# Optimization experiments

Hardware: AMD Instinct MI355X
Metric: run time of the kernel (lower is better)

The kernel has to match this reference:

```python
import jax, jax.numpy as jnp
import numpy as np

NUM_HEADS = 4
DIM_MODEL = 256
DIM_HEAD = DIM_MODEL // NUM_HEADS  # 64


def _conv1x1(w, b, x):
    # Conv1d kernel_size=1: [B, D_in, N] -> [B, D_out, N]
    return jnp.einsum('oi,bin->bon', w, x) + b[None, :, None]


def setup_inputs() -> dict:
    key = jax.random.key(0)
    ks = jax.random.split(key, 12)
    B, D, N = 8, DIM_MODEL, 2048
    s = 1.0 / np.sqrt(D)
    inp = {
        'query': jax.random.normal(ks[0], (B, D, N), dtype=jnp.float32),
        'key': jax.random.normal(ks[1], (B, D, N), dtype=jnp.float32),
        'value': jax.random.normal(ks[2], (B, D, N), dtype=jnp.float32),
        'wq': jax.random.normal(ks[3], (D, D), dtype=jnp.float32) * s,
        'bq': jax.random.normal(ks[4], (D,), dtype=jnp.float32) * 0.01,
        'wk': jax.random.normal(ks[5], (D, D), dtype=jnp.float32) * s,
        'bk': jax.random.normal(ks[6], (D,), dtype=jnp.float32) * 0.01,
        'wv': jax.random.normal(ks[7], (D, D), dtype=jnp.float32) * s,
        'bv': jax.random.normal(ks[8], (D,), dtype=jnp.float32) * 0.01,
        'wm': jax.random.normal(ks[9], (D, D), dtype=jnp.float32) * s,
        'bm': jax.random.normal(ks[10], (D,), dtype=jnp.float32) * 0.01,
    }
    return inp


def reference(query, key, value, wq, bq, wk, bk, wv, bv, wm, bm):
    B = query.shape[0]
    d, h = DIM_HEAD, NUM_HEADS
    # 1x1 conv projections, then split channels as (dim_head, num_heads) per torch view
    q = _conv1x1(wq, bq, query).reshape(B, d, h, -1)  # [B, d, h, N]
    k = _conv1x1(wk, bk, key).reshape(B, d, h, -1)    # [B, d, h, M]
    v = _conv1x1(wv, bv, value).reshape(B, d, h, -1)  # [B, d, h, M]
    norm = 1.0 / float(d) ** 0.5
    scores = jnp.einsum('bdhn,bdhm->bhnm', q, k) * norm  # [B, h, N, M]
    prob = jax.nn.softmax(scores, axis=-1)
    attn = jnp.einsum('bhnm,bdhm->bdhn', prob, v)        # [B, d, h, N]
    out = _conv1x1(wm, bm, attn.reshape(B, d * h, -1))   # [B, D, N]
    return out
```

## Files before the change

kernel.cpp:

```cpp
#include <hip/hip_runtime.h>
#include <math.h>

#define BB 8
#define DD 256
#define NN 2048
#define NH 4
#define DH 64

typedef _Float16 half8   __attribute__((ext_vector_type(8)));
typedef _Float16 half4_t __attribute__((ext_vector_type(4)));
typedef _Float16 half2_t __attribute__((ext_vector_type(2)));
typedef float    floatx4 __attribute__((ext_vector_type(4)));

#define MFMA32(A, B, C) __builtin_amdgcn_mfma_f32_16x16x32_f16(A, B, C, 0, 0, 0)

#define SC 0.18033688011112042f

__global__ __launch_bounds__(256) void prep_weights(
    const float* __restrict__ wq, const float* __restrict__ wk,
    const float* __restrict__ wv, const float* __restrict__ wm,
    _Float16* __restrict__ wqf, _Float16* __restrict__ wkf,
    _Float16* __restrict__ wvf, _Float16* __restrict__ wmf)
{
    int id = blockIdx.x * 256 + threadIdx.x;
    wqf[id] = (_Float16)wq[id];
    wkf[id] = (_Float16)wk[id];
    wvf[id] = (_Float16)wv[id];
    int row = id >> 8, col = id & 255;
    int hh = col >> 6, dd = col & 63;
    wmf[id] = (_Float16)wm[row * 256 + dd * 4 + hh];
}


__global__ __launch_bounds__(256, 3) void conv_qkv(
    const _Float16* __restrict__ wqf, const _Float16* __restrict__ wkf,
    const _Float16* __restrict__ wvf,
    const float* __restrict__ bq, const float* __restrict__ bk,
    const float* __restrict__ bv,
    const float* __restrict__ Xq, const float* __restrict__ Xk,
    const float* __restrict__ Xv,
    _Float16* __restrict__ Yq, _Float16* __restrict__ Yk,
    _Float16* __restrict__ Yv)
{
    const int n0 = blockIdx.x * 64;
    const int b  = blockIdx.y;
    const int zh = blockIdx.z;
    const int z  = zh >> 1;
    const int hf = zh & 1;
    const _Float16* Wf = z == 0 ? wqf : (z == 1 ? wkf : wvf);
    const float* bias  = z == 0 ? bq  : (z == 1 ? bk  : bv);
    const float* X     = z == 0 ? Xq  : (z == 1 ? Xk  : Xv);
    const float osc    = z == 0 ? SC : 1.0f;
    const int cout0 = hf * 128;

    const int t = threadIdx.x;
    const int w = t >> 6, l = t & 63, c = l & 15, q = l >> 4;

    __shared__ _Float16 smem[64 * 264];

    half8 af[2][8];
    {
        const _Float16* wp = Wf + (size_t)(cout0 + w * 32 + c) * 256 + q * 8;
        #pragma unroll
        for (int rt = 0; rt < 2; ++rt)
            #pragma unroll
            for (int ch = 0; ch < 8; ++ch)
                af[rt][ch] = *(const half8*)(wp + rt * 16 * 256 + ch * 32);
    }

    {
        const int nb = t & 15, kb = t >> 4;
        #pragma unroll
        for (int cc = 0; cc < 4; ++cc) {
            const float* Xg = X + (size_t)b * DD * NN +
                              (size_t)(cc * 64 + kb * 4) * NN + n0 + nb * 4;
            float4 x[4];
            #pragma unroll
            for (int i = 0; i < 4; ++i) x[i] = *(const float4*)(Xg + (size_t)i * NN);
            #pragma unroll
            for (int j = 0; j < 4; ++j) {
                half4_t hv;
                #pragma unroll
                for (int i = 0; i < 4; ++i) hv[i] = (_Float16)(((const float*)&x[i])[j]);
                *(half4_t*)(smem + (nb * 4 + j) * 264 + cc * 64 + kb * 4) = hv;
            }
        }
    }
    __syncthreads();

    floatx4 acc[2][4];
    #pragma unroll
    for (int rt = 0; rt < 2; ++rt)
        #pragma unroll
        for (int nt = 0; nt < 4; ++nt) acc[rt][nt] = (floatx4){0.f, 0.f, 0.f, 0.f};

    #pragma unroll
    for (int ch = 0; ch < 8; ++ch)
        #pragma unroll
        for (int nt = 0; nt < 4; ++nt) {
            half8 bx = *(const half8*)(smem + (nt * 16 + c) * 264 + ch * 32 + q * 8);
            acc[0][nt] = MFMA32(af[0][ch], bx, acc[0][nt]);
            acc[1][nt] = MFMA32(af[1][ch], bx, acc[1][nt]);
        }

    if (z < 2) {
        __syncthreads();
        #pragma unroll
        for (int rt = 0; rt < 2; ++rt)
            #pragma unroll
            for (int nt = 0; nt < 4; ++nt) {
                half4_t hv;
                #pragma unroll
                for (int r = 0; r < 4; ++r)
                    hv[r] = (_Float16)((acc[rt][nt][r] +
                            bias[cout0 + w * 32 + rt * 16 + q * 4 + r]) * osc);
                *(half4_t*)(smem + (nt * 16 + c) * 136 + w * 32 + rt * 16 + q * 4) = hv;
            }
        __syncthreads();
        _Float16* Y = z == 0 ? Yq : Yk;
        const int nn = t >> 2, hh = t & 3;
        half8 hv[4];
        #pragma unroll
        for (int i = 0; i < 4; ++i)
            #pragma unroll
            for (int k = 0; k < 8; ++k)
                hv[i][k] = smem[nn * 136 + (i * 8 + k) * 4 + hh];
        _Float16* dst = Y + ((size_t)(b * NH + hh) * NN + n0 + nn) * 64 + hf * 32;
        #pragma unroll
        for (int i = 0; i < 4; ++i) *(half8*)(dst + i * 8) = hv[i];
    } else {
        __syncthreads();
        #pragma unroll
        for (int rt = 0; rt < 2; ++rt)
            #pragma unroll
            for (int nt = 0; nt < 4; ++nt)
                #pragma unroll
                for (int r = 0; r < 4; ++r)
                    smem[(w * 32 + rt * 16 + q * 4 + r) * 72 + nt * 16 + c] =
                        (_Float16)(acc[rt][nt][r] +
                                   bias[cout0 + w * 32 + rt * 16 + q * 4 + r]);
        __syncthreads();
        const int cl = t >> 1, noff = (t & 1) * 32;
        const int cout = cout0 + cl;
        const int hh = cout & 3, dd = cout >> 2;
        _Float16* dst = Yv + ((size_t)(b * NH + hh) * 64 + dd) * NN + n0 + noff;
        #pragma unroll
        for (int i = 0; i < 4; ++i)
            *(half8*)(dst + i * 8) = *(const half8*)(smem + cl * 72 + noff + i * 8);
    }
}

__global__ __launch_bounds__(256, 3) void conv_o(
    const _Float16* __restrict__ Wf, const float* __restrict__ bias,
    const _Float16* __restrict__ At, float* __restrict__ out)
{
    const int n0 = blockIdx.x * 64;
    const int b  = blockIdx.y;
    const int hf = blockIdx.z;
    const int cout0 = hf * 128;

    const int t = threadIdx.x;
    const int w = t >> 6, l = t & 63, c = l & 15, q = l >> 4;

    __shared__ float fs[128 * 66];

    half8 af[2][8];
    {
        const _Float16* wp = Wf + (size_t)(cout0 + w * 32 + c) * 256 + q * 8;
        #pragma unroll
        for (int rt = 0; rt < 2; ++rt)
            #pragma unroll
            for (int ch = 0; ch < 8; ++ch)
                af[rt][ch] = *(const half8*)(wp + rt * 16 * 256 + ch * 32);
    }

    floatx4 acc[2][4];
    #pragma unroll
    for (int rt = 0; rt < 2; ++rt)
        #pragma unroll
        for (int nt = 0; nt < 4; ++nt) acc[rt][nt] = (floatx4){0.f, 0.f, 0.f, 0.f};

    #pragma unroll
    for (int ch = 0; ch < 8; ++ch)
        #pragma unroll
        for (int nt = 0; nt < 4; ++nt) {
            half8 bx = *(const half8*)(At +
                ((size_t)b * NN + n0 + nt * 16 + c) * 256 + ch * 32 + q * 8);
            acc[0][nt] = MFMA32(af[0][ch], bx, acc[0][nt]);
            acc[1][nt] = MFMA32(af[1][ch], bx, acc[1][nt]);
        }

    #pragma unroll
    for (int rt = 0; rt < 2; ++rt)
        #pragma unroll
        for (int nt = 0; nt < 4; ++nt)
            #pragma unroll
            for (int r = 0; r < 4; ++r)
                fs[(w * 32 + rt * 16 + q * 4 + r) * 66 + nt * 16 + c] =
                    acc[rt][nt][r] + bias[cout0 + w * 32 + rt * 16 + q * 4 + r];
    __syncthreads();
    const int cl = t >> 1, noff = (t & 1) * 32;
    float* dst = out + (size_t)b * DD * NN + (size_t)(cout0 + cl) * NN + n0 + noff;
    #pragma unroll
    for (int i = 0; i < 8; ++i)
        *(float4*)(dst + i * 4) = *(const float4*)(fs + cl * 66 + noff + i * 4);
}

__global__ __launch_bounds__(512) void attn_mfma6(
    const _Float16* __restrict__ Qt, const _Float16* __restrict__ Kt,
    const _Float16* __restrict__ V, _Float16* __restrict__ At)
{
    const int n0 = blockIdx.x * 128;
    const int h  = blockIdx.y;
    const int b  = blockIdx.z;
    const int t  = threadIdx.x;
    const int w  = t >> 6, l = t & 63, c = l & 15, q = l >> 4;

    const size_t bh = (size_t)(b * NH + h);

    __shared__ _Float16 smem[9216 + 8704];
    _Float16* Ks = smem;
    _Float16* Vs = smem + 9216;

    half8 bq2[2];
    #pragma unroll
    for (int ch = 0; ch < 2; ++ch)
        bq2[ch] = *(const half8*)(Qt + (bh * NN + n0 + w * 16 + c) * 64 + ch * 32 + q * 8);

    float lp = 0.f;
    floatx4 o[4];
    #pragma unroll
    for (int dt = 0; dt < 4; ++dt) o[dt] = (floatx4){0.f, 0.f, 0.f, 0.f};

    const int ksr = t >> 2, ksc = (t & 3) * 16;
    const int vr  = t >> 3, vcb = (t & 7) * 16;
    const _Float16* Kg = Kt + bh * NN * 64;
    const _Float16* Vg = V + bh * 64 * NN;

    half8 kpre[2], vpre[2];
    kpre[0] = *(const half8*)(Kg + (size_t)ksr * 64 + ksc);
    kpre[1] = *(const half8*)(Kg + (size_t)ksr * 64 + ksc + 8);
    vpre[0] = *(const half8*)(Vg + (size_t)vr * NN + vcb);
    vpre[1] = *(const half8*)(Vg + (size_t)vr * NN + vcb + 8);

    for (int m0 = 0; m0 < NN; m0 += 128) {
        __syncthreads();
        *(half8*)(Ks + ksr * 72 + ksc)     = kpre[0];
        *(half8*)(Ks + ksr * 72 + ksc + 8) = kpre[1];
        #pragma unroll
        for (int u = 0; u < 2; ++u) {
            const int mb = vcb + u * 8;
            const int p0 = (mb & ~31) + (((mb >> 2) & 3) << 3) + (((mb >> 4) & 1) << 2);
            half4_t lo, hi;
            #pragma unroll
            for (int j = 0; j < 4; ++j) { lo[j] = vpre[u][j]; hi[j] = vpre[u][4 + j]; }
            *(half4_t*)(Vs + vr * 136 + p0)     = lo;
            *(half4_t*)(Vs + vr * 136 + p0 + 8) = hi;
        }
        __syncthreads();

        const int mn = (m0 + 128 < NN) ? m0 + 128 : m0;
        kpre[0] = *(const half8*)(Kg + (size_t)(mn + ksr) * 64 + ksc);
        kpre[1] = *(const half8*)(Kg + (size_t)(mn + ksr) * 64 + ksc + 8);
        vpre[0] = *(const half8*)(Vg + (size_t)vr * NN + mn + vcb);
        vpre[1] = *(const half8*)(Vg + (size_t)vr * NN + mn + vcb + 8);

        #pragma unroll
        for (int mt2 = 0; mt2 < 4; ++mt2) {
            half8 p8;
            #pragma unroll
            for (int hfm = 0; hfm < 2; ++hfm) {
                const int mt = mt2 * 2 + hfm;
                floatx4 s = {0.f, 0.f, 0.f, 0.f};
                #pragma unroll
                for (int ch = 0; ch < 2; ++ch) {
                    half8 ak = *(const half8*)(Ks + (mt * 16 + c) * 72 + ch * 32 + q * 8);
                    s = MFMA32(ak, bq2[ch], s);
                }
                float e0 = exp2f(s[0]), e1 = exp2f(s[1]);
                float e2 = exp2f(s[2]), e3 = exp2f(s[3]);
                lp += (e0 + e1) + (e2 + e3);
                half2_t c01 = __builtin_bit_cast(half2_t, __builtin_amdgcn_cvt_pkrtz(e0, e1));
                half2_t c23 = __builtin_bit_cast(half2_t, __builtin_amdgcn_cvt_pkrtz(e2, e3));
                p8[hfm * 4 + 0] = c01[0]; p8[hfm * 4 + 1] = c01[1];
                p8[hfm * 4 + 2] = c23[0]; p8[hfm * 4 + 3] = c23[1];
            }
            #pragma unroll
            for (int dt = 0; dt < 4; ++dt) {
                half8 av = *(const half8*)(Vs + (dt * 16 + c) * 136 + mt2 * 32 + q * 8);
                o[dt] = MFMA32(av, p8, o[dt]);
            }
        }
    }

    lp += __shfl_xor(lp, 16);
    lp += __shfl_xor(lp, 32);
    const float inv = 1.f / lp;

    __syncthreads();
    _Float16* fsm = smem;
    #pragma unroll
    for (int dt = 0; dt < 4; ++dt) {
        half4_t hv;
        #pragma unroll
        for (int r = 0; r < 4; ++r) hv[r] = (_Float16)(o[dt][r] * inv);
        *(half4_t*)(fsm + (w * 16 + c) * 72 + dt * 16 + q * 4) = hv;
    }
    __syncthreads();
    const int rn = t >> 2, seg = (t & 3) * 16;
    _Float16* dst = At + ((size_t)b * NN + n0 + rn) * 256 + h * 64 + seg;
    *(half8*)(dst)     = *(const half8*)(fsm + rn * 72 + seg);
    *(half8*)(dst + 8) = *(const half8*)(fsm + rn * 72 + seg + 8);
}

extern "C" void kernel_launch(void* const* d_in, const int* in_sizes, int n_in,
                              void* d_out, int out_size, void* d_ws, size_t ws_size,
                              hipStream_t stream) {
    const float* query = (const float*)d_in[0];
    const float* key_  = (const float*)d_in[1];
    const float* value = (const float*)d_in[2];
    const float* wq    = (const float*)d_in[3];
    const float* bq    = (const float*)d_in[4];
    const float* wk    = (const float*)d_in[5];
    const float* bk    = (const float*)d_in[6];
    const float* wv    = (const float*)d_in[7];
    const float* bv    = (const float*)d_in[8];
    const float* wm    = (const float*)d_in[9];
    const float* bm    = (const float*)d_in[10];
    float* out = (float*)d_out;

    _Float16* ws = (_Float16*)d_ws;
    _Float16* wqf = ws;
    _Float16* wkf = wqf + 65536;
    _Float16* wvf = wkf + 65536;
    _Float16* wmf = wvf + 65536;
    const size_t e16 = (size_t)BB * NH * NN * DH;
    _Float16* qf = ws + 262144;
    _Float16* kf = qf + e16;
    _Float16* vf = kf + e16;
    _Float16* at = vf + e16;

    prep_weights<<<256, 256, 0, stream>>>(wq, wk, wv, wm, wqf, wkf, wvf, wmf);
    conv_qkv<<<dim3(32, 8, 6), 256, 0, stream>>>(wqf, wkf, wvf, bq, bk, bv,
                                                 query, key_, value, qf, kf, vf);
    attn_mfma6<<<dim3(16, 4, 8), 512, 0, stream>>>(qf, kf, vf, at);
    conv_o<<<dim3(32, 8, 2), 256, 0, stream>>>(wmf, bm, at, out);
}
```

Baseline: 199.1 us.

## Double-buffer attention K/V tiles, swizzle LDS, merge conv_qkv output halves

The attention kernel now double-buffers K/V tiles in shared memory, so each iteration needs one barrier instead of two and staging of the next tile overlaps compute. LDS layouts for K, V and the conv input tile get XOR swizzles to cut bank conflicts on the MFMA operand reads. conv_qkv has each block compute both 128-channel output halves from one staged input tile, halving the input loads and conversions at the cost of half as many blocks. The doubled shared memory in attention may lower occupancy.

Measured after the change: 202.0 us. About the same (+1.5%).

```diff
diff --git a/kernel.cpp b/kernel.cpp
--- a/kernel.cpp
+++ b/kernel.cpp
@@ -31,7 +31,6 @@
     wmf[id] = (_Float16)wm[row * 256 + dd * 4 + hh];
 }
 
-
 __global__ __launch_bounds__(256, 3) void conv_qkv(
     const _Float16* __restrict__ wqf, const _Float16* __restrict__ wkf,
     const _Float16* __restrict__ wvf,
@@ -44,32 +43,24 @@
 {
     const int n0 = blockIdx.x * 64;
     const int b  = blockIdx.y;
-    const int zh = blockIdx.z;
-    const int z  = zh >> 1;
-    const int hf = zh & 1;
+    const int z  = blockIdx.z;
     const _Float16* Wf = z == 0 ? wqf : (z == 1 ? wkf : wvf);
     const float* bias  = z == 0 ? bq  : (z == 1 ? bk  : bv);
     const float* X     = z == 0 ? Xq  : (z == 1 ? Xk  : Xv);
     const float osc    = z == 0 ? SC : 1.0f;
-    const int cout0 = hf * 128;
 
     const int t = threadIdx.x;
     const int w = t >> 6, l = t & 63, c = l & 15, q = l >> 4;
 
-    __shared__ _Float16 smem[64 * 264];
-
-    half8 af[2][8];
-    {
-        const _Float16* wp = Wf + (size_t)(cout0 + w * 32 + c) * 256 + q * 8;
-        #pragma unroll
-        for (int rt = 0; rt < 2; ++rt)
-            #pragma unroll
-            for (int ch = 0; ch < 8; ++ch)
-                af[rt][ch] = *(const half8*)(wp + rt * 16 * 256 + ch * 32);
-    }
+    __shared__ _Float16 smem[64 * 264 + 9216];
+    _Float16* Xs = smem;
+    _Float16* Es = smem + 64 * 264;
+
+    const int gk = (c & 3) << 1;
 
     {
         const int nb = t & 15, kb = t >> 4;
+        const int slot = (kb >> 1), sub = (kb & 1) * 4;
         #pragma unroll
         for (int cc = 0; cc < 4; ++cc) {
             const float* Xg = X + (size_t)b * DD * NN +
@@ -82,71 +73,87 @@
                 half4_t hv;
                 #pragma unroll
                 for (int i = 0; i < 4; ++i) hv[i] = (_Float16)(((const float*)&x[i])[j]);
-                *(half4_t*)(smem + (nb * 4 + j) * 264 + cc * 64 + kb * 4) = hv;
+                *(half4_t*)(Xs + (nb * 4 + j) * 264 +
+                            (((cc * 8 + slot) ^ (j << 1)) << 3) + sub) = hv;
             }
         }
     }
     __syncthreads();
 
-    floatx4 acc[2][4];
-    #pragma unroll
-    for (int rt = 0; rt < 2; ++rt)
-        #pragma unroll
-        for (int nt = 0; nt < 4; ++nt) acc[rt][nt] = (floatx4){0.f, 0.f, 0.f, 0.f};
-
-    #pragma unroll
-    for (int ch = 0; ch < 8; ++ch)
-        #pragma unroll
-        for (int nt = 0; nt < 4; ++nt) {
-            half8 bx = *(const half8*)(smem + (nt * 16 + c) * 264 + ch * 32 + q * 8);
-            acc[0][nt] = MFMA32(af[0][ch], bx, acc[0][nt]);
-            acc[1][nt] = MFMA32(af[1][ch], bx, acc[1][nt]);
-        }
-
-    if (z < 2) {
-        __syncthreads();
+    for (int hf = 0; hf < 2; ++hf) {
+        const int cout0 = hf * 128;
+
+        half8 af[2][8];
+        {
+            const _Float16* wp = Wf + (size_t)(cout0 + w * 32 + c) * 256 + q * 8;
+            #pragma unroll
+            for (int rt = 0; rt < 2; ++rt)
+                #pragma unroll
+                for (int ch = 0; ch < 8; ++ch)
+                    af[rt][ch] = *(const half8*)(wp + rt * 16 * 256 + ch * 32);
+        }
+
+        floatx4 acc[2][4];
         #pragma unroll
         for (int rt = 0; rt < 2; ++rt)
             #pragma unroll
+            for (int nt = 0; nt < 4; ++nt) acc[rt][nt] = (floatx4){0.f, 0.f, 0.f, 0.f};
+
+        #pragma unroll
+        for (int ch = 0; ch < 8; ++ch)
+            #pragma unroll
             for (int nt = 0; nt < 4; ++nt) {
-                half4_t hv;
-                #pragma unroll
-                for (int r = 0; r < 4; ++r)
-                    hv[r] = (_Float16)((acc[rt][nt][r] +
-                            bias[cout0 + w * 32 + rt * 16 + q * 4 + r]) * osc);
-                *(half4_t*)(smem + (nt * 16 + c) * 136 + w * 32 + rt * 16 + q * 4) = hv;
+                half8 bx = *(const half8*)(Xs + (nt * 16 + c) * 264 +
+                                           (((ch * 4 + q) ^ gk) << 3));
+                acc[0][nt] = MFMA32(af[0][ch], bx, acc[0][nt]);
+                acc[1][nt] = MFMA32(af[1][ch], bx, acc[1][nt]);
             }
-        __syncthreads();
-        _Float16* Y = z == 0 ? Yq : Yk;
-        const int nn = t >> 2, hh = t & 3;
-        half8 hv[4];
-        #pragma unroll
-        for (int i = 0; i < 4; ++i)
-            #pragma unroll
-            for (int k = 0; k < 8; ++k)
-                hv[i][k] = smem[nn * 136 + (i * 8 + k) * 4 + hh];
-        _Float16* dst = Y + ((size_t)(b * NH + hh) * NN + n0 + nn) * 64 + hf * 32;
-        #pragma unroll
-        for (int i = 0; i < 4; ++i) *(half8*)(dst + i * 8) = hv[i];
-    } else {
-        __syncthreads();
-        #pragma unroll
-        for (int rt = 0; rt < 2; ++rt)
-            #pragma unroll
-            for (int nt = 0; nt < 4; ++nt)
-                #pragma unroll
-                for (int r = 0; r < 4; ++r)
-                    smem[(w * 32 + rt * 16 + q * 4 + r) * 72 + nt * 16 + c] =
-                        (_Float16)(acc[rt][nt][r] +
-                                   bias[cout0 + w * 32 + rt * 16 + q * 4 + r]);
-        __syncthreads();
-        const int cl = t >> 1, noff = (t & 1) * 32;
-        const int cout = cout0 + cl;
-        const int hh = cout & 3, dd = cout >> 2;
-        _Float16* dst = Yv + ((size_t)(b * NH + hh) * 64 + dd) * NN + n0 + noff;
-        #pragma unroll
-        for (int i = 0; i < 4; ++i)
-            *(half8*)(dst + i * 8) = *(const half8*)(smem + cl * 72 + noff + i * 8);
+
+        if (z < 2) {
+            __syncthreads();
+            #pragma unroll
+            for (int rt = 0; rt < 2; ++rt)
+                #pragma unroll
+                for (int nt = 0; nt < 4; ++nt) {
+                    half4_t hv;
+                    #pragma unroll
+                    for (int r = 0; r < 4; ++r)
+                        hv[r] = (_Float16)((acc[rt][nt][r] +
+                                bias[cout0 + w * 32 + rt * 16 + q * 4 + r]) * osc);
+                    *(half4_t*)(Es + (nt * 16 + c) * 136 + w * 32 + rt * 16 + q * 4) = hv;
+                }
+            __syncthreads();
+            _Float16* Y = z == 0 ? Yq : Yk;
+            const int nn = t >> 2, hh = t & 3;
+            half8 hv[4];
+            #pragma unroll
+            for (int i = 0; i < 4; ++i)
+                #pragma unroll
+                for (int k = 0; k < 8; ++k)
+                    hv[i][k] = Es[nn * 136 + (i * 8 + k) * 4 + hh];
+            _Float16* dst = Y + ((size_t)(b * NH + hh) * NN + n0 + nn) * 64 + hf * 32;
+            #pragma unroll
+            for (int i = 0; i < 4; ++i) *(half8*)(dst + i * 8) = hv[i];
+        } else {
+            __syncthreads();
+            #pragma unroll
+            for (int rt = 0; rt < 2; ++rt)
+                #pragma unroll
+                for (int nt = 0; nt < 4; ++nt)
+                    #pragma unroll
+                    for (int r = 0; r < 4; ++r)
+                        Es[(w * 32 + rt * 16 + q * 4 + r) * 72 + nt * 16 + c] =
+                            (_Float16)(acc[rt][nt][r] +
+                                       bias[cout0 + w * 32 + rt * 16 + q * 4 + r]);
+            __syncthreads();
+            const int cl = t >> 1, noff = (t & 1) * 32;
+            const int cout = cout0 + cl;
+            const int hh = cout & 3, dd = cout >> 2;
+            _Float16* dst = Yv + ((size_t)(b * NH + hh) * 64 + dd) * NN + n0 + noff;
+            #pragma unroll
+            for (int i = 0; i < 4; ++i)
+                *(half8*)(dst + i * 8) = *(const half8*)(Es + cl * 72 + noff + i * 8);
+        }
     }
 }
 
@@ -218,9 +225,7 @@
 
     const size_t bh = (size_t)(b * NH + h);
 
-    __shared__ _Float16 smem[9216 + 8704];
-    _Float16* Ks = smem;
-    _Float16* Vs = smem + 9216;
+    __shared__ _Float16 smem[2 * 17920];
 
     half8 bq2[2];
     #pragma unroll
@@ -236,6 +241,18 @@
     const int vr  = t >> 3, vcb = (t & 7) * 16;
     const _Float16* Kg = Kt + bh * NN * 64;
     const _Float16* Vg = V + bh * 64 * NN;
+
+    const int gk  = (c & 3) << 1;
+    const int rk0 = ((0 + q) ^ gk) << 3;
+    const int rk1 = ((4 + q) ^ gk) << 3;
+    int rv[4];
+    #pragma unroll
+    for (int mt2 = 0; mt2 < 4; ++mt2) rv[mt2] = ((mt2 * 4 + q) ^ gk) << 3;
+    const int gK  = (ksr & 3) << 1;
+    const int s0  = (t & 3) * 2;
+    const int wk0 = (s0 ^ gK) << 3;
+    const int wk1 = ((s0 + 1) ^ gK) << 3;
+    const int gV  = (vr & 3) << 1;
 
     half8 kpre[2], vpre[2];
     kpre[0] = *(const half8*)(Kg + (size_t)ksr * 64 + ksc);
@@ -243,28 +260,46 @@
     vpre[0] = *(const half8*)(Vg + (size_t)vr * NN + vcb);
     vpre[1] = *(const half8*)(Vg + (size_t)vr * NN + vcb + 8);
 
-    for (int m0 = 0; m0 < NN; m0 += 128) {
-        __syncthreads();
-        *(half8*)(Ks + ksr * 72 + ksc)     = kpre[0];
-        *(half8*)(Ks + ksr * 72 + ksc + 8) = kpre[1];
-        #pragma unroll
-        for (int u = 0; u < 2; ++u) {
-            const int mb = vcb + u * 8;
-            const int p0 = (mb & ~31) + (((mb >> 2) & 3) << 3) + (((mb >> 4) & 1) << 2);
-            half4_t lo, hi;
-            #pragma unroll
-            for (int j = 0; j < 4; ++j) { lo[j] = vpre[u][j]; hi[j] = vpre[u][4 + j]; }
-            *(half4_t*)(Vs + vr * 136 + p0)     = lo;
-            *(half4_t*)(Vs + vr * 136 + p0 + 8) = hi;
-        }
-        __syncthreads();
-
-        const int mn = (m0 + 128 < NN) ? m0 + 128 : m0;
-        kpre[0] = *(const half8*)(Kg + (size_t)(mn + ksr) * 64 + ksc);
-        kpre[1] = *(const half8*)(Kg + (size_t)(mn + ksr) * 64 + ksc + 8);
-        vpre[0] = *(const half8*)(Vg + (size_t)vr * NN + mn + vcb);
-        vpre[1] = *(const half8*)(Vg + (size_t)vr * NN + mn + vcb + 8);
-
+#define STAGE_TILE(KSP, VSP)                                                    \
+    {                                                                           \
+        *(half8*)((KSP) + ksr * 72 + wk0) = kpre[0];                            \
+        *(half8*)((KSP) + ksr * 72 + wk1) = kpre[1];                            \
+        _Pragma("unroll")                                                       \
+        for (int u = 0; u < 2; ++u) {                                           \
+            const int mb = vcb + u * 8;                                         \
+            const int p0 = (mb & ~31) + (((mb >> 2) & 3) << 3) +                \
+                           (((mb >> 4) & 1) << 2);                              \
+            const int sl = p0 >> 3, sub = p0 & 7;                               \
+            half4_t lo, hi;                                                     \
+            _Pragma("unroll")                                                   \
+            for (int j = 0; j < 4; ++j) { lo[j] = vpre[u][j]; hi[j] = vpre[u][4 + j]; } \
+            *(half4_t*)((VSP) + vr * 136 + ((sl ^ gV) << 3) + sub)       = lo;  \
+            *(half4_t*)((VSP) + vr * 136 + (((sl + 1) ^ gV) << 3) + sub) = hi;  \
+        }                                                                       \
+    }
+
+    STAGE_TILE(smem, smem + 9216);
+    kpre[0] = *(const half8*)(Kg + (size_t)(128 + ksr) * 64 + ksc);
+    kpre[1] = *(const half8*)(Kg + (size_t)(128 + ksr) * 64 + ksc + 8);
+    vpre[0] = *(const half8*)(Vg + (size_t)vr * NN + 128 + vcb);
+    vpre[1] = *(const half8*)(Vg + (size_t)vr * NN + 128 + vcb + 8);
+    __syncthreads();
+
+    for (int it = 0; it < 16; ++it) {
+        if (it < 15) {
+            _Float16* Ksw = smem + ((it + 1) & 1) * 17920;
+            _Float16* Vsw = Ksw + 9216;
+            STAGE_TILE(Ksw, Vsw);
+        }
+        {
+            const int mn = (it + 2 < 16) ? (it + 2) * 128 : it * 128;
+            kpre[0] = *(const half8*)(Kg + (size_t)(mn + ksr) * 64 + ksc);
+            kpre[1] = *(const half8*)(Kg + (size_t)(mn + ksr) * 64 + ksc + 8);
+            vpre[0] = *(const half8*)(Vg + (size_t)vr * NN + mn + vcb);
+            vpre[1] = *(const half8*)(Vg + (size_t)vr * NN + mn + vcb + 8);
+        }
+        const _Float16* Ks = smem + (it & 1) * 17920;
+        const _Float16* Vs = Ks + 9216;
         #pragma unroll
         for (int mt2 = 0; mt2 < 4; ++mt2) {
             half8 p8;
@@ -272,11 +307,10 @@
             for (int hfm = 0; hfm < 2; ++hfm) {
                 const int mt = mt2 * 2 + hfm;
                 floatx4 s = {0.f, 0.f, 0.f, 0.f};
-                #pragma unroll
-                for (int ch = 0; ch < 2; ++ch) {
-                    half8 ak = *(const half8*)(Ks + (mt * 16 + c) * 72 + ch * 32 + q * 8);
-                    s = MFMA32(ak, bq2[ch], s);
-                }
+                half8 ak0 = *(const half8*)(Ks + (mt * 16 + c) * 72 + rk0);
+                s = MFMA32(ak0, bq2[0], s);
+                half8 ak1 = *(const half8*)(Ks + (mt * 16 + c) * 72 + rk1);
+                s = MFMA32(ak1, bq2[1], s);
                 float e0 = exp2f(s[0]), e1 = exp2f(s[1]);
                 float e2 = exp2f(s[2]), e3 = exp2f(s[3]);
                 lp += (e0 + e1) + (e2 + e3);
@@ -287,17 +321,18 @@
             }
             #pragma unroll
             for (int dt = 0; dt < 4; ++dt) {
-                half8 av = *(const half8*)(Vs + (dt * 16 + c) * 136 + mt2 * 32 + q * 8);
+                half8 av = *(const half8*)(Vs + (dt * 16 + c) * 136 + rv[mt2]);
                 o[dt] = MFMA32(av, p8, o[dt]);
             }
         }
-    }
+        __syncthreads();
+    }
+#undef STAGE_TILE
 
     lp += __shfl_xor(lp, 16);
     lp += __shfl_xor(lp, 32);
     const float inv = 1.f / lp;
 
-    __syncthreads();
     _Float16* fsm = smem;
     #pragma unroll
     for (int dt = 0; dt < 4; ++dt) {
@@ -341,7 +376,7 @@
     _Float16* at = vf + e16;
 
     prep_weights<<<256, 256, 0, stream>>>(wq, wk, wv, wm, wqf, wkf, wvf, wmf);
-    conv_qkv<<<dim3(32, 8, 6), 256, 0, stream>>>(wqf, wkf, wvf, bq, bk, bv,
+    conv_qkv<<<dim3(32, 8, 3), 256, 0, stream>>>(wqf, wkf, wvf, bq, bk, bv,
                                                  query, key_, value, qf, kf, vf);
     attn_mfma6<<<dim3(16, 4, 8), 512, 0, stream>>>(qf, kf, vf, at);
     conv_o<<<dim3(32, 8, 2), 256, 0, stream>>>(wmf, bm, at, out);
```
